# Kernel tuning notes

Hardware: AMD Instinct MI355X
Metric: run time of the kernel (lower is better)

The kernel has to match this reference:

```python
import jax, jax.numpy as jnp
import numpy as np

B, T, C, H = 4, 2048, 2048, 16
HD = C // H  # head_size = 128
EPS = 1e-5


def layernorm(x, g, b):
    mu = jnp.mean(x, axis=-1, keepdims=True)
    var = jnp.var(x, axis=-1, keepdims=True)
    return (x - mu) * jax.lax.rsqrt(var + EPS) * g + b


def setup_inputs() -> dict:
    key = jax.random.key(0)
    ks = jax.random.split(key, 12)
    s_attn = 1.0 / np.sqrt(C)
    s_ffn1 = 1.0 / np.sqrt(C)
    s_ffn2 = 1.0 / np.sqrt(4 * C)
    return {
        "x": jax.random.normal(ks[0], (B, T, C), jnp.float32),
        "Wq": jax.random.normal(ks[1], (H, C, HD), jnp.float32) * s_attn,
        "Wk": jax.random.normal(ks[2], (H, C, HD), jnp.float32) * s_attn,
        "Wv": jax.random.normal(ks[3], (H, C, HD), jnp.float32) * s_attn,
        "Wp": jax.random.normal(ks[4], (C, C), jnp.float32) * s_attn,
        "bp": jnp.zeros((C,), jnp.float32),
        "W1": jax.random.normal(ks[5], (C, 4 * C), jnp.float32) * s_ffn1,
        "b1": jnp.zeros((4 * C,), jnp.float32),
        "W2": jax.random.normal(ks[6], (4 * C, C), jnp.float32) * s_ffn2,
        "b2": jnp.zeros((C,), jnp.float32),
        "g1": jnp.ones((C,), jnp.float32),
        "beta1": jnp.zeros((C,), jnp.float32),
        "g2": jnp.ones((C,), jnp.float32),
        "beta2": jnp.zeros((C,), jnp.float32),
    }


def reference(x, Wq, Wk, Wv, Wp, bp, W1, b1, W2, b2, g1, beta1, g2, beta2):
    # --- attention sublayer (pre-LN, causal) ---
    h = layernorm(x, g1, beta1)
    q = jnp.einsum("btc,hcd->bhtd", h, Wq)
    k = jnp.einsum("bsc,hcd->bhsd", h, Wk)
    v = jnp.einsum("bsc,hcd->bhsd", h, Wv)
    scores = jnp.einsum("bhtd,bhsd->bhts", q, k) / jnp.sqrt(jnp.asarray(HD, x.dtype))
    causal = jnp.tril(jnp.ones((T, T), bool))
    scores = jnp.where(causal, scores, jnp.asarray(-jnp.inf, x.dtype))
    w = jax.nn.softmax(scores, axis=-1)  # dropout = identity (eval mode)
    o = jnp.einsum("bhts,bhsd->bhtd", w, v)
    o = o.transpose(0, 2, 1, 3).reshape(B, T, C)  # concat heads
    x = x + o @ Wp + bp
    # --- feed-forward sublayer ---
    h2 = layernorm(x, g2, beta2)
    f = jax.nn.gelu(h2 @ W1 + b1, approximate=False)
    x = x + f @ W2 + b2
    return x
```

## Files before the change

kernel.cpp:

```cpp
#include <hip/hip_runtime.h>
#include <math.h>

#define B_ 4
#define T_ 2048
#define C_ 2048
#define H_ 16
#define HD_ 128

typedef __attribute__((ext_vector_type(8))) short short8;
typedef __attribute__((ext_vector_type(4))) float f32x4;
typedef unsigned short u16;
typedef unsigned int u32;

__device__ __forceinline__ u16 f2bf(float f) {
  union { float f; unsigned u; } v; v.f = f;
  unsigned r = v.u + 0x7FFFu + ((v.u >> 16) & 1u);
  return (u16)(r >> 16);
}

__device__ __forceinline__ u16 f2bf_trunc(float f) {
  union { float f; unsigned u; } v; v.f = f;
  return (u16)(v.u >> 16);
}

__device__ __forceinline__ void gld16(const void* g, void* l) {
  __builtin_amdgcn_global_load_lds(
      (__attribute__((address_space(1))) void*)(void*)g,
      (__attribute__((address_space(3))) void*)l, 16, 0, 0);
}

__global__ __launch_bounds__(256) void tconv(const float* __restrict__ in,
                                             u16* __restrict__ out,
                                             int K, int N,
                                             long inBS, long outBS) {
  __shared__ float tile[32][33];
  const float* inb = in + (long)blockIdx.z * inBS;
  u16* outb = out + (long)blockIdx.z * outBS;
  int k0 = blockIdx.x << 5, n0 = blockIdx.y << 5;
  int t = threadIdx.x;
  {
    int kk = t >> 3, nn = (t & 7) << 2;
    float4 v = *(const float4*)(inb + (long)(k0 + kk) * N + n0 + nn);
    tile[kk][nn + 0] = v.x; tile[kk][nn + 1] = v.y;
    tile[kk][nn + 2] = v.z; tile[kk][nn + 3] = v.w;
  }
  __syncthreads();
  {
    int nn = t >> 3, kk = (t & 7) << 2;
    ushort4 o;
    o.x = f2bf(tile[kk + 0][nn]); o.y = f2bf(tile[kk + 1][nn]);
    o.z = f2bf(tile[kk + 2][nn]); o.w = f2bf(tile[kk + 3][nn]);
    *(ushort4*)(outb + (long)(n0 + nn) * K + k0 + kk) = o;
  }
}

__global__ __launch_bounds__(256) void ln_rows(const float* __restrict__ x,
                                               const float* __restrict__ gam,
                                               const float* __restrict__ bet,
                                               u16* __restrict__ out) {
  int row = blockIdx.x;
  const float* xr = x + (size_t)row * C_;
  int t = threadIdx.x;
  float4 v0 = *(const float4*)(xr + t * 8);
  float4 v1 = *(const float4*)(xr + t * 8 + 4);
  float s = v0.x + v0.y + v0.z + v0.w + v1.x + v1.y + v1.z + v1.w;
  float ss = v0.x * v0.x + v0.y * v0.y + v0.z * v0.z + v0.w * v0.w +
             v1.x * v1.x + v1.y * v1.y + v1.z * v1.z + v1.w * v1.w;
  for (int d = 32; d > 0; d >>= 1) {
    s += __shfl_down(s, d);
    ss += __shfl_down(ss, d);
  }
  __shared__ float red[8];
  int wv = t >> 6;
  if ((t & 63) == 0) { red[wv] = s; red[4 + wv] = ss; }
  __syncthreads();
  s = red[0] + red[1] + red[2] + red[3];
  ss = red[4] + red[5] + red[6] + red[7];
  float mu = s * (1.0f / C_);
  float var = ss * (1.0f / C_) - mu * mu;
  float rs = rsqrtf(var + 1e-5f);
  int c = t * 8;
  float vv[8] = {v0.x, v0.y, v0.z, v0.w, v1.x, v1.y, v1.z, v1.w};
  ushort4 o0, o1;
  o0.x = f2bf((vv[0] - mu) * rs * gam[c + 0] + bet[c + 0]);
  o0.y = f2bf((vv[1] - mu) * rs * gam[c + 1] + bet[c + 1]);
  o0.z = f2bf((vv[2] - mu) * rs * gam[c + 2] + bet[c + 2]);
  o0.w = f2bf((vv[3] - mu) * rs * gam[c + 3] + bet[c + 3]);
  o1.x = f2bf((vv[4] - mu) * rs * gam[c + 4] + bet[c + 4]);
  o1.y = f2bf((vv[5] - mu) * rs * gam[c + 5] + bet[c + 5]);
  o1.z = f2bf((vv[6] - mu) * rs * gam[c + 6] + bet[c + 6]);
  o1.w = f2bf((vv[7] - mu) * rs * gam[c + 7] + bet[c + 7]);
  *(ushort4*)(out + (size_t)row * C_ + c) = o0;
  *(ushort4*)(out + (size_t)row * C_ + c + 4) = o1;
}

template <int EPI>
__global__ __launch_bounds__(512, 2) void gemm256(
    const u16* __restrict__ A, const u16* __restrict__ BT,
    int M, int N, int K, int lda, int ldb,
    u16* __restrict__ oq, u16* __restrict__ ok, u16* __restrict__ ovt,
    float* __restrict__ of32, const float* __restrict__ resid,
    const float* __restrict__ bias, u16* __restrict__ obf, int addBias) {
  extern __shared__ char smem[];
  int nbx = N >> 8;
  int nwg = gridDim.x;
  int flat = blockIdx.x;
  int sw = (flat & 7) * (nwg >> 3) + (flat >> 3);
  int bx = sw % nbx, by = sw / nbx;
  int m0 = by << 8, n0 = bx << 8;
  int tid = threadIdx.x;
  int lane = tid & 63, wave = tid >> 6;
  int wm = wave >> 2, wn = wave & 3;
  int l15 = lane & 15, l16 = lane >> 4;
  int nt = K >> 6;

  f32x4 acc[8][4] = {};
  short8 afA[4][2], afB[4][2], bfA[2][2], bfB[2][2];

  auto stage = [&](int b, int r, int k0) {
    int row = (r & 3) * 64 + (tid >> 3);
    int lslot = (tid & 7) ^ (row & 7);
    char* dst = smem + ((r < 4) ? 0 : 65536) + b * 32768 + (r & 3) * 8192 + tid * 16;
    const u16* src = ((r < 4) ? (A + (long)(m0 + row) * lda)
                              : (BT + (long)(n0 + row) * ldb)) +
                     k0 + lslot * 8;
    gld16(src, dst);
  };
  auto ldA = [&](int cur, int mf, int kk) {
    int row = wm * 128 + mf * 16 + l15;
    int slot = (kk * 4 + l16) ^ (row & 7);
    return *(const short8*)(smem + cur * 32768 + row * 128 + slot * 16);
  };
  auto ldB = [&](int cur, int nf, int kk) {
    int row = wn * 64 + nf * 16 + l15;
    int slot = (kk * 4 + l16) ^ (row & 7);
    return *(const short8*)(smem + 65536 + cur * 32768 + row * 128 + slot * 16);
  };

#pragma unroll
  for (int r = 0; r < 8; ++r) stage(0, r, 0);
  __syncthreads();

#pragma unroll
  for (int mq = 0; mq < 4; ++mq)
#pragma unroll
    for (int kk = 0; kk < 2; ++kk) afA[mq][kk] = ldA(0, mq, kk);
#pragma unroll
  for (int nq = 0; nq < 2; ++nq)
#pragma unroll
    for (int kk = 0; kk < 2; ++kk) bfA[nq][kk] = ldB(0, nq, kk);

  for (int t = 0; t < nt; ++t) {
    int cur = t & 1, nxt = cur ^ 1;
    bool more = (t + 1) < nt;
    int k1 = (t + 1) << 6;
    if (more) {
#pragma unroll
      for (int r = 0; r < 8; ++r) stage(nxt, r, k1);
    }
#pragma unroll
    for (int nq = 0; nq < 2; ++nq)
#pragma unroll
      for (int kk = 0; kk < 2; ++kk) bfB[nq][kk] = ldB(cur, 2 + nq, kk);
    __builtin_amdgcn_s_setprio(1);
#pragma unroll
    for (int mq = 0; mq < 4; ++mq)
#pragma unroll
      for (int nq = 0; nq < 2; ++nq)
#pragma unroll
        for (int kk = 0; kk < 2; ++kk)
          acc[mq][nq] = __builtin_amdgcn_mfma_f32_16x16x32_bf16(
              afA[mq][kk], bfA[nq][kk], acc[mq][nq], 0, 0, 0);
    __builtin_amdgcn_s_setprio(0);
#pragma unroll
    for (int mq = 0; mq < 4; ++mq)
#pragma unroll
      for (int kk = 0; kk < 2; ++kk) afB[mq][kk] = ldA(cur, 4 + mq, kk);
    __builtin_amdgcn_s_setprio(1);
#pragma unroll
    for (int mq = 0; mq < 4; ++mq)
#pragma unroll
      for (int nq = 0; nq < 2; ++nq)
#pragma unroll
        for (int kk = 0; kk < 2; ++kk)
          acc[mq][2 + nq] = __builtin_amdgcn_mfma_f32_16x16x32_bf16(
              afA[mq][kk], bfB[nq][kk], acc[mq][2 + nq], 0, 0, 0);
    __builtin_amdgcn_s_setprio(0);
    __builtin_amdgcn_s_setprio(1);
#pragma unroll
    for (int mq = 0; mq < 4; ++mq)
#pragma unroll
      for (int nq = 0; nq < 2; ++nq)
#pragma unroll
        for (int kk = 0; kk < 2; ++kk)
          acc[4 + mq][nq] = __builtin_amdgcn_mfma_f32_16x16x32_bf16(
              afB[mq][kk], bfA[nq][kk], acc[4 + mq][nq], 0, 0, 0);
    __builtin_amdgcn_s_setprio(0);
    __builtin_amdgcn_s_setprio(1);
#pragma unroll
    for (int mq = 0; mq < 4; ++mq)
#pragma unroll
      for (int nq = 0; nq < 2; ++nq)
#pragma unroll
        for (int kk = 0; kk < 2; ++kk)
          acc[4 + mq][2 + nq] = __builtin_amdgcn_mfma_f32_16x16x32_bf16(
              afB[mq][kk], bfB[nq][kk], acc[4 + mq][2 + nq], 0, 0, 0);
    __builtin_amdgcn_s_setprio(0);
    if (more) {
      __syncthreads();
#pragma unroll
      for (int mq = 0; mq < 4; ++mq)
#pragma unroll
        for (int kk = 0; kk < 2; ++kk) afA[mq][kk] = ldA(nxt, mq, kk);
#pragma unroll
      for (int nq = 0; nq < 2; ++nq)
#pragma unroll
        for (int kk = 0; kk < 2; ++kk) bfA[nq][kk] = ldB(nxt, nq, kk);
    }
  }

#pragma unroll
  for (int mf = 0; mf < 8; ++mf) {
#pragma unroll
    for (int nf = 0; nf < 4; ++nf) {
      int rowf = m0 + wm * 128 + mf * 16 + l16 * 4;
      int col = n0 + wn * 64 + nf * 16 + l15;
      if constexpr (EPI == 0) {
        int seg = col >> 11, cn = col & 2047;
        int hh = cn >> 7, dd = cn & 127;
        int bb = rowf >> 11, t0 = rowf & 2047;
        if (seg == 2) {
          ushort4 o;
          o.x = f2bf(acc[mf][nf][0]); o.y = f2bf(acc[mf][nf][1]);
          o.z = f2bf(acc[mf][nf][2]); o.w = f2bf(acc[mf][nf][3]);
          *(ushort4*)(ovt + ((long)(bb * H_ + hh) * HD_ + dd) * T_ + t0) = o;
        } else if (seg == 0) {
          const float qs = 0.08838834764831845f * 1.4426950408889634f;
#pragma unroll
          for (int r = 0; r < 4; ++r)
            oq[((long)(bb * H_ + hh) * T_ + t0 + r) * HD_ + dd] =
                f2bf(acc[mf][nf][r] * qs);
        } else {
#pragma unroll
          for (int r = 0; r < 4; ++r)
            ok[((long)(bb * H_ + hh) * T_ + t0 + r) * HD_ + dd] =
                f2bf(acc[mf][nf][r]);
        }
      } else if constexpr (EPI == 1) {
#pragma unroll
        for (int r = 0; r < 4; ++r) {
          long idx = (long)(rowf + r) * N + col;
          of32[idx] = resid[idx] + bias[col] + acc[mf][nf][r];
        }
      } else if constexpr (EPI == 2) {
#pragma unroll
        for (int r = 0; r < 4; ++r) {
          float v = acc[mf][nf][r] + bias[col];
          float g = 0.5f * v * (1.0f + erff(v * 0.70710678118654752f));
          obf[(long)(rowf + r) * N + col] = f2bf(g);
        }
      } else {
#pragma unroll
        for (int r = 0; r < 4; ++r) {
          long idx = (long)(rowf + r) * N + col;
          float v = acc[mf][nf][r];
          if (addBias) v += bias[col];
          of32[idx] += v;
        }
      }
    }
  }
}

__global__ __launch_bounds__(256) void attn_fwd(const u16* __restrict__ q,
                                                const u16* __restrict__ k,
                                                const u16* __restrict__ vt,
                                                u16* __restrict__ o) {
  extern __shared__ char asmem[];
  int bid = blockIdx.x;
  int bh = bid & 63;
  int qb = 31 - (bid >> 6);
  int q0 = qb << 6;
  int tid = threadIdx.x, lane = tid & 63, wave = tid >> 6;
  int l15 = lane & 15, l16 = lane >> 4;
  int wq0 = q0 + wave * 16;
  const u16* kbase = k + (long)bh * T_ * HD_;
  const u16* vbase = vt + (long)bh * HD_ * T_;
  char* Psw = asmem + 32768 + wave * 1024;

  short8 qf[4];
#pragma unroll
  for (int kk = 0; kk < 4; ++kk)
    qf[kk] = *(const short8*)(q + ((long)bh * T_ + wq0 + l15) * HD_ +
                              kk * 32 + l16 * 8);

  short8 vone;
#pragma unroll
  for (int j = 0; j < 8; ++j) vone[j] = (short)0x3F80;

  f32x4 accO[8] = {};
  float m_r[4], l_r[4];
#pragma unroll
  for (int r = 0; r < 4; ++r) { m_r[r] = -INFINITY; l_r[r] = 0.f; }

  int nt = 2 * qb + 2;

  auto stage = [&](int b, int t) {
    int s0 = t << 5;
    char* Kd = asmem + b * 8192;
    char* Vd = asmem + 16384 + b * 8192;
#pragma unroll
    for (int r = 0; r < 2; ++r) {
      int off = r * 4096 + tid * 16;
      int krow = off >> 8;
      int kslot = (tid & 15) ^ (krow & 7);
      gld16(kbase + (long)(s0 + krow) * HD_ + kslot * 8, Kd + off);
      int dd = off >> 6;
      int vslot = (tid & 3) ^ (dd & 3);
      gld16(vbase + (long)dd * T_ + s0 + vslot * 8, Vd + off);
    }
  };

  stage(0, 0);
  asm volatile("s_waitcnt vmcnt(0)" ::: "memory");
  __syncthreads();

  for (int t = 0; t < nt; ++t) {
    int s0 = t << 5;
    int cur = t & 1;
    bool more = (t + 1 < nt);
    if (more) stage(cur ^ 1, t + 1);

    if (s0 <= wq0 + 15) {
      const char* Kc = asmem + cur * 8192;
      const char* Vc = asmem + 16384 + cur * 8192;
      bool needmask = (s0 + 31 > wq0);
      f32x4 S[2];
#pragma unroll
      for (int sb = 0; sb < 2; ++sb) {
        f32x4 s = {};
#pragma unroll
        for (int kk = 0; kk < 4; ++kk) {
          int srow = sb * 16 + l15;
          int kb = srow * 256 + (((kk * 4 + l16) ^ (srow & 7)) << 4);
          short8 kf = *(const short8*)(Kc + kb);
          s = __builtin_amdgcn_mfma_f32_16x16x32_bf16(qf[kk], kf, s, 0, 0, 0);
        }
        S[sb] = s;
      }
      float mxl[4];
      bool growL = false;
#pragma unroll
      for (int r = 0; r < 4; ++r) {
        int tt = wq0 + 4 * l16 + r;
        float mx = -INFINITY;
#pragma unroll
        for (int sb = 0; sb < 2; ++sb) {
          float v = S[sb][r];
          if (needmask && (s0 + sb * 16 + l15 > tt)) v = -INFINITY;
          S[sb][r] = v;
          mx = fmaxf(mx, v);
        }
        mxl[r] = mx;
        growL = growL || (mx > m_r[r] + 8.0f);
      }
      bool anyg = __any(growL);
      float al[4];
      if (anyg) {
#pragma unroll
        for (int r = 0; r < 4; ++r) {
          float mx = mxl[r];
          mx = fmaxf(mx, __shfl_xor(mx, 1));
          mx = fmaxf(mx, __shfl_xor(mx, 2));
          mx = fmaxf(mx, __shfl_xor(mx, 4));
          mx = fmaxf(mx, __shfl_xor(mx, 8));
          float mo = m_r[r];
          float mn = fmaxf(mo, mx);
          al[r] = exp2f(mo - mn);
          m_r[r] = mn;
        }
      } else {
#pragma unroll
        for (int r = 0; r < 4; ++r) al[r] = 1.0f;
      }
#pragma unroll
      for (int r = 0; r < 4; ++r) {
        float mn = m_r[r];
        int prow = 4 * l16 + r;
#pragma unroll
        for (int sb = 0; sb < 2; ++sb) {
          float p = exp2f(S[sb][r] - mn);
          int col = sb * 16 + l15;
          int slot = col >> 3;
          int pb = prow * 64 + ((slot ^ l16) << 4) + (col & 7) * 2;
          *(u16*)(Psw + pb) = f2bf_trunc(p);
        }
      }
      if (anyg) {
#pragma unroll
        for (int db = 0; db < 8; ++db)
#pragma unroll
          for (int r = 0; r < 4; ++r) accO[db][r] *= al[r];
      }
      int pslot = l16 ^ ((l15 >> 2) & 3);
      short8 pf = *(const short8*)(Psw + l15 * 64 + (pslot << 4));
      f32x4 zz = {};
      f32x4 sacc = __builtin_amdgcn_mfma_f32_16x16x32_bf16(pf, vone, zz, 0, 0, 0);
#pragma unroll
      for (int r = 0; r < 4; ++r) l_r[r] = l_r[r] * al[r] + sacc[r];
#pragma unroll
      for (int db = 0; db < 8; ++db) {
        int vrow = db * 16 + l15;
        int vb = vrow * 64 + ((l16 ^ (vrow & 3)) << 4);
        short8 vf = *(const short8*)(Vc + vb);
        accO[db] = __builtin_amdgcn_mfma_f32_16x16x32_bf16(pf, vf,
                                                           accO[db], 0, 0, 0);
      }
    }
    if (more) asm volatile("s_waitcnt vmcnt(0)" ::: "memory");
    __syncthreads();
  }

  int bb = bh >> 4, hh = bh & 15;
  float inv[4];
#pragma unroll
  for (int r = 0; r < 4; ++r) inv[r] = 1.0f / l_r[r];
#pragma unroll
  for (int db = 0; db < 8; ++db)
#pragma unroll
    for (int r = 0; r < 4; ++r) {
      int tt = wq0 + 4 * l16 + r;
      o[((long)bb * T_ + tt) * C_ + hh * HD_ + db * 16 + l15] =
          f2bf(accO[db][r] * inv[r]);
    }
}

extern "C" void kernel_launch(void* const* d_in, const int* in_sizes, int n_in,
                              void* d_out, int out_size, void* d_ws, size_t ws_size,
                              hipStream_t stream) {
  (void)in_sizes; (void)n_in; (void)out_size; (void)ws_size;
  const float* x   = (const float*)d_in[0];
  const float* Wq  = (const float*)d_in[1];
  const float* Wk  = (const float*)d_in[2];
  const float* Wv  = (const float*)d_in[3];
  const float* Wp  = (const float*)d_in[4];
  const float* bp  = (const float*)d_in[5];
  const float* W1  = (const float*)d_in[6];
  const float* b1  = (const float*)d_in[7];
  const float* W2  = (const float*)d_in[8];
  const float* b2  = (const float*)d_in[9];
  const float* g1  = (const float*)d_in[10];
  const float* be1 = (const float*)d_in[11];
  const float* g2  = (const float*)d_in[12];
  const float* be2 = (const float*)d_in[13];
  float* out = (float*)d_out;

  (void)hipFuncSetAttribute((const void*)gemm256<0>,
                            hipFuncAttributeMaxDynamicSharedMemorySize, 131072);
  (void)hipFuncSetAttribute((const void*)gemm256<1>,
                            hipFuncAttributeMaxDynamicSharedMemorySize, 131072);
  (void)hipFuncSetAttribute((const void*)gemm256<2>,
                            hipFuncAttributeMaxDynamicSharedMemorySize, 131072);
  (void)hipFuncSetAttribute((const void*)gemm256<3>,
                            hipFuncAttributeMaxDynamicSharedMemorySize, 131072);
  (void)hipFuncSetAttribute((const void*)attn_fwd,
                            hipFuncAttributeMaxDynamicSharedMemorySize, 36864);

  char* ws = (char*)d_ws;
  size_t off = 0;
  auto alloc = [&](size_t n) {
    void* p = ws + off;
    off += (n + 255) & ~(size_t)255;
    return p;
  };
  u16* wqkvT = (u16*)alloc((size_t)6144 * 2048 * 2);
  u16* wpT   = (u16*)alloc((size_t)2048 * 2048 * 2);
  u16* w1T   = (u16*)alloc((size_t)8192 * 2048 * 2);
  u16* w2T   = (u16*)alloc((size_t)2048 * 8192 * 2);
  u16* hb    = (u16*)alloc((size_t)8192 * 2048 * 2);
  u16* qbuf  = (u16*)alloc((size_t)8192 * 2048 * 2);
  u16* kbuf  = (u16*)alloc((size_t)8192 * 2048 * 2);
  u16* vtbuf = (u16*)alloc((size_t)8192 * 2048 * 2);
  u16* ob = hb;
  u16* fb = qbuf;

  tconv<<<dim3(64, 4, 16), 256, 0, stream>>>(Wq, wqkvT, 2048, 128,
                                             (long)2048 * 128, (long)128 * 2048);
  tconv<<<dim3(64, 4, 16), 256, 0, stream>>>(Wk, wqkvT + (size_t)2048 * 2048, 2048, 128,
                                             (long)2048 * 128, (long)128 * 2048);
  tconv<<<dim3(64, 4, 16), 256, 0, stream>>>(Wv, wqkvT + (size_t)4096 * 2048, 2048, 128,
                                             (long)2048 * 128, (long)128 * 2048);
  tconv<<<dim3(64, 64, 1), 256, 0, stream>>>(Wp, wpT, 2048, 2048, 0, 0);
  tconv<<<dim3(64, 256, 1), 256, 0, stream>>>(W1, w1T, 2048, 8192, 0, 0);
  tconv<<<dim3(256, 64, 1), 256, 0, stream>>>(W2, w2T, 8192, 2048, 0, 0);

  ln_rows<<<8192, 256, 0, stream>>>(x, g1, be1, hb);
  gemm256<0><<<768, 512, 131072, stream>>>(hb, wqkvT, 8192, 6144, 2048, 2048, 2048,
                                           qbuf, kbuf, vtbuf, nullptr, nullptr,
                                           nullptr, nullptr, 0);
  attn_fwd<<<2048, 256, 36864, stream>>>(qbuf, kbuf, vtbuf, ob);
  gemm256<1><<<256, 512, 131072, stream>>>(ob, wpT, 8192, 2048, 2048, 2048, 2048,
                                           nullptr, nullptr, nullptr, out, x, bp,
                                           nullptr, 0);

  ln_rows<<<8192, 256, 0, stream>>>(out, g2, be2, hb);
  for (int c = 0; c < 2; ++c) {
    gemm256<2><<<512, 512, 131072, stream>>>(hb, w1T + (size_t)c * 4096 * 2048,
                                             8192, 4096, 2048, 2048, 2048,
                                             nullptr, nullptr, nullptr, nullptr,
                                             nullptr, b1 + c * 4096, fb, 0);
    gemm256<3><<<256, 512, 131072, stream>>>(fb, w2T + (size_t)c * 4096,
                                             8192, 2048, 4096, 4096, 8192,
                                             nullptr, nullptr, nullptr, out,
                                             nullptr, b2, nullptr, c == 0 ? 1 : 0);
  }
}
```

Measured before the change: 1.083 ms.

## Split GEMM k-tile into two k-halves with partial vmcnt waits

Reorganizes the shared-memory layout of the 256x256x64 GEMM tile into two 32-wide k-slabs with a new XOR swizzle. Loads are reordered so each k-half lands separately, and the code waits with explicit vmcnt counts plus raw barriers instead of a full __syncthreads. The goal is to start MFMAs on the first k-half while the second is still in flight and to cut register pressure from the four fragment sets. Correctness now depends on the hand-counted vmcnt values matching the order in which global-to-LDS loads are issued.

```diff
diff --git a/kernel.cpp b/kernel.cpp
--- a/kernel.cpp
+++ b/kernel.cpp
@@ -115,40 +115,38 @@
   int nt = K >> 6;
 
   f32x4 acc[8][4] = {};
-  short8 afA[4][2], afB[4][2], bfA[2][2], bfB[2][2];
+  short8 af[8], bf[4];
 
   auto stage = [&](int b, int r, int k0) {
-    int row = (r & 3) * 64 + (tid >> 3);
-    int lslot = (tid & 7) ^ (row & 7);
-    char* dst = smem + ((r < 4) ? 0 : 65536) + b * 32768 + (r & 3) * 8192 + tid * 16;
-    const u16* src = ((r < 4) ? (A + (long)(m0 + row) * lda)
-                              : (BT + (long)(n0 + row) * ldb)) +
-                     k0 + lslot * 8;
+    int isB = (r >> 1) & 1;
+    int ks = r >> 2;
+    int row = (r & 1) * 128 + (tid >> 2);
+    int swz = (row & 3) ^ ((row >> 2) & 3);
+    int gslot = (tid & 3) ^ swz;
+    char* dst = smem + isB * 65536 + b * 32768 + ks * 16384 + (r & 1) * 8192 +
+                tid * 16;
+    const u16* src = (isB ? (BT + (long)(n0 + row) * ldb)
+                          : (A + (long)(m0 + row) * lda)) +
+                     k0 + ks * 32 + gslot * 8;
     gld16(src, dst);
   };
-  auto ldA = [&](int cur, int mf, int kk) {
+  auto ldA = [&](int b, int ks, int mf) {
     int row = wm * 128 + mf * 16 + l15;
-    int slot = (kk * 4 + l16) ^ (row & 7);
-    return *(const short8*)(smem + cur * 32768 + row * 128 + slot * 16);
+    int swz = (row & 3) ^ ((row >> 2) & 3);
+    return *(const short8*)(smem + b * 32768 + ks * 16384 + row * 64 +
+                            ((l16 ^ swz) << 4));
   };
-  auto ldB = [&](int cur, int nf, int kk) {
+  auto ldB = [&](int b, int ks, int nf) {
     int row = wn * 64 + nf * 16 + l15;
-    int slot = (kk * 4 + l16) ^ (row & 7);
-    return *(const short8*)(smem + 65536 + cur * 32768 + row * 128 + slot * 16);
+    int swz = (row & 3) ^ ((row >> 2) & 3);
+    return *(const short8*)(smem + 65536 + b * 32768 + ks * 16384 + row * 64 +
+                            ((l16 ^ swz) << 4));
   };
 
 #pragma unroll
   for (int r = 0; r < 8; ++r) stage(0, r, 0);
-  __syncthreads();
-
-#pragma unroll
-  for (int mq = 0; mq < 4; ++mq)
-#pragma unroll
-    for (int kk = 0; kk < 2; ++kk) afA[mq][kk] = ldA(0, mq, kk);
-#pragma unroll
-  for (int nq = 0; nq < 2; ++nq)
-#pragma unroll
-    for (int kk = 0; kk < 2; ++kk) bfA[nq][kk] = ldB(0, nq, kk);
+  asm volatile("s_waitcnt vmcnt(4)" ::: "memory");
+  __builtin_amdgcn_s_barrier();
 
   for (int t = 0; t < nt; ++t) {
     int cur = t & 1, nxt = cur ^ 1;
@@ -159,63 +157,37 @@
       for (int r = 0; r < 8; ++r) stage(nxt, r, k1);
     }
 #pragma unroll
-    for (int nq = 0; nq < 2; ++nq)
-#pragma unroll
-      for (int kk = 0; kk < 2; ++kk) bfB[nq][kk] = ldB(cur, 2 + nq, kk);
+    for (int mf = 0; mf < 8; ++mf) af[mf] = ldA(cur, 0, mf);
+#pragma unroll
+    for (int nf = 0; nf < 4; ++nf) bf[nf] = ldB(cur, 0, nf);
     __builtin_amdgcn_s_setprio(1);
 #pragma unroll
-    for (int mq = 0; mq < 4; ++mq)
-#pragma unroll
-      for (int nq = 0; nq < 2; ++nq)
-#pragma unroll
-        for (int kk = 0; kk < 2; ++kk)
-          acc[mq][nq] = __builtin_amdgcn_mfma_f32_16x16x32_bf16(
-              afA[mq][kk], bfA[nq][kk], acc[mq][nq], 0, 0, 0);
+    for (int mf = 0; mf < 8; ++mf)
+#pragma unroll
+      for (int nf = 0; nf < 4; ++nf)
+        acc[mf][nf] = __builtin_amdgcn_mfma_f32_16x16x32_bf16(
+            af[mf], bf[nf], acc[mf][nf], 0, 0, 0);
     __builtin_amdgcn_s_setprio(0);
-#pragma unroll
-    for (int mq = 0; mq < 4; ++mq)
-#pragma unroll
-      for (int kk = 0; kk < 2; ++kk) afB[mq][kk] = ldA(cur, 4 + mq, kk);
+    if (more)
+      asm volatile("s_waitcnt vmcnt(8)" ::: "memory");
+    else
+      asm volatile("s_waitcnt vmcnt(0)" ::: "memory");
+    __builtin_amdgcn_s_barrier();
+#pragma unroll
+    for (int mf = 0; mf < 8; ++mf) af[mf] = ldA(cur, 1, mf);
+#pragma unroll
+    for (int nf = 0; nf < 4; ++nf) bf[nf] = ldB(cur, 1, nf);
     __builtin_amdgcn_s_setprio(1);
 #pragma unroll
-    for (int mq = 0; mq < 4; ++mq)
-#pragma unroll
-      for (int nq = 0; nq < 2; ++nq)
-#pragma unroll
-        for (int kk = 0; kk < 2; ++kk)
-          acc[mq][2 + nq] = __builtin_amdgcn_mfma_f32_16x16x32_bf16(
-              afA[mq][kk], bfB[nq][kk], acc[mq][2 + nq], 0, 0, 0);
-    __builtin_amdgcn_s_setprio(0);
-    __builtin_amdgcn_s_setprio(1);
-#pragma unroll
-    for (int mq = 0; mq < 4; ++mq)
-#pragma unroll
-      for (int nq = 0; nq < 2; ++nq)
-#pragma unroll
-        for (int kk = 0; kk < 2; ++kk)
-          acc[4 + mq][nq] = __builtin_amdgcn_mfma_f32_16x16x32_bf16(
-              afB[mq][kk], bfA[nq][kk], acc[4 + mq][nq], 0, 0, 0);
-    __builtin_amdgcn_s_setprio(0);
-    __builtin_amdgcn_s_setprio(1);
-#pragma unroll
-    for (int mq = 0; mq < 4; ++mq)
-#pragma unroll
-      for (int nq = 0; nq < 2; ++nq)
-#pragma unroll
-        for (int kk = 0; kk < 2; ++kk)
-          acc[4 + mq][2 + nq] = __builtin_amdgcn_mfma_f32_16x16x32_bf16(
-              afB[mq][kk], bfB[nq][kk], acc[4 + mq][2 + nq], 0, 0, 0);
+    for (int mf = 0; mf < 8; ++mf)
+#pragma unroll
+      for (int nf = 0; nf < 4; ++nf)
+        acc[mf][nf] = __builtin_amdgcn_mfma_f32_16x16x32_bf16(
+            af[mf], bf[nf], acc[mf][nf], 0, 0, 0);
     __builtin_amdgcn_s_setprio(0);
     if (more) {
-      __syncthreads();
-#pragma unroll
-      for (int mq = 0; mq < 4; ++mq)
-#pragma unroll
-        for (int kk = 0; kk < 2; ++kk) afA[mq][kk] = ldA(nxt, mq, kk);
-#pragma unroll
-      for (int nq = 0; nq < 2; ++nq)
-#pragma unroll
-        for (int kk = 0; kk < 2; ++kk) bfA[nq][kk] = ldB(nxt, nq, kk);
+      asm volatile("s_waitcnt vmcnt(4)" ::: "memory");
+      __builtin_amdgcn_s_barrier();
     }
   }
 
```

Measured after the change: 1.252 ms. 1.16x slower.
